# Kernel optimization log

Measured on AMD Instinct MI355X. Metric: run time of the kernel, lower is better.

The kernel has to match this reference:

```python
import jax, jax.numpy as jnp
import numpy as np

B, S, D, H = 4, 2048, 1024, 16
DH = D // H


def setup_inputs() -> dict:
    key = jax.random.key(0)
    kq, kk, kv, kw, kb = jax.random.split(key, 5)
    queries = jax.random.normal(kq, (B, S, D), dtype=jnp.float32)
    keys = jax.random.normal(kk, (B, S, D), dtype=jnp.float32)
    values = jax.random.normal(kv, (B, S, D), dtype=jnp.float32)
    # True = masked-out padding position; mask the last 64 keys of batch 0
    kpm = np.zeros((B, S), dtype=bool)
    kpm[0, -64:] = True
    key_padding_mask = jnp.asarray(kpm)
    W_O = jax.random.normal(kw, (D, D), dtype=jnp.float32) / np.sqrt(D)
    b_O = jax.random.normal(kb, (D,), dtype=jnp.float32) * 0.01
    return {"queries": queries, "keys": keys, "values": values,
            "key_padding_mask": key_padding_mask, "W_O": W_O, "b_O": b_O}


def reference(queries, keys, values, key_padding_mask, W_O, b_O):
    batch, len_q, d_model = queries.shape
    len_k = keys.shape[1]
    # [B, H, S, DH]
    q = queries.reshape(batch, len_q, H, DH).transpose(0, 2, 1, 3)
    k = keys.reshape(batch, len_k, H, DH).transpose(0, 2, 1, 3)
    v = values.reshape(batch, len_k, H, DH).transpose(0, 2, 1, 3)
    sim = jnp.einsum('bhqd,bhkd->bhqk', q, k) / jnp.sqrt(jnp.float32(DH))
    neg_inf = jnp.finfo(sim.dtype).min
    # padding mask: True means masked
    sim = jnp.where(key_padding_mask[:, None, None, :], neg_inf, sim)
    # causal mask (is_causal=True)
    causal = jnp.tril(jnp.ones((len_q, len_k), dtype=bool))
    sim = jnp.where(causal[None, None], sim, neg_inf)
    attn = jax.nn.softmax(sim, axis=-1)
    out = jnp.einsum('bhqk,bhkd->bhqd', attn, v)  # [B, H, Sq, DH]
    out = out.transpose(0, 2, 1, 3).reshape(batch, len_q, d_model)
    return out @ W_O.T + b_O
```

## Files before the change

### kernel.cpp

```cpp
#include <hip/hip_runtime.h>
#include <hip/hip_bf16.h>

#define B_ 4
#define S_ 2048
#define D_ 1024
#define H_ 16
#define DH_ 64

typedef __attribute__((ext_vector_type(8))) short bf16x8;
typedef __attribute__((ext_vector_type(4))) float f32x4;
typedef __attribute__((ext_vector_type(16))) float f32x16;
typedef __attribute__((ext_vector_type(2))) int v2i;
typedef unsigned int uint32;

__device__ __forceinline__ unsigned short f2bf(float f) {
  unsigned int u = __float_as_uint(f);
  u += 0x7FFFu + ((u >> 16) & 1u);
  return (unsigned short)(u >> 16);
}

__device__ __forceinline__ uint32 pk2(float lo, float hi) {
  return __builtin_amdgcn_perm(__float_as_uint(hi), __float_as_uint(lo), 0x07060302u);
}

__device__ __forceinline__ float half_add(float v) {
  v2i r = __builtin_amdgcn_permlane32_swap(__float_as_int(v), __float_as_int(v), false, false);
  return __int_as_float(r[0]) + __int_as_float(r[1]);
}

__global__ void prep_kernel(const float* __restrict__ k, const float* __restrict__ w,
                            const int* __restrict__ kpm, const float* __restrict__ v,
                            ushort* __restrict__ Kb, ushort* __restrict__ Wb,
                            float* __restrict__ MF, int* __restrict__ anyM,
                            ushort* __restrict__ Vt) {
  __shared__ ushort tile[64][68];
  const int bid = blockIdx.x;
  const int t = threadIdx.x;
  if (bid < 8192) {
    int i = bid * 256 + t;
    float4 a = ((const float4*)k)[i];
    ushort4 r;
    r.x = f2bf(a.x); r.y = f2bf(a.y); r.z = f2bf(a.z); r.w = f2bf(a.w);
    ((ushort4*)Kb)[i] = r;
  } else if (bid < 9216) {
    int i = (bid - 8192) * 256 + t;
    float4 a = ((const float4*)w)[i];
    ushort4 r;
    r.x = f2bf(a.x); r.y = f2bf(a.y); r.z = f2bf(a.z); r.w = f2bf(a.w);
    ((ushort4*)Wb)[i] = r;
  } else if (bid < 9248) {
    int i = (bid - 9216) * 256 + t;
    int m = kpm[i];
    MF[i] = m ? -1e30f : 0.0f;
    unsigned long long bal = __ballot(m != 0);
    if ((i & 63) == 0) anyM[i >> 6] = (bal != 0ull) ? 1 : 0;
  } else {
    int bx = bid - 9248;
    int bh = bx >> 5;
    int s0 = (bx & 31) << 6;
    int b = bh >> 4, h = bh & 15;
#pragma unroll
    for (int it = 0; it < 16; ++it) {
      int r = it * 4 + (t >> 6);
      int c = t & 63;
      float x = v[(size_t)(b * S_ + s0 + r) * D_ + h * DH_ + c];
      tile[r][c] = f2bf(x);
    }
    __syncthreads();
#pragma unroll
    for (int it = 0; it < 16; ++it) {
      int d = it * 4 + (t >> 6);
      int s = t & 63;
      Vt[(size_t)(bh * DH_ + d) * S_ + s0 + s] = tile[s][d];
    }
  }
}

__global__ __launch_bounds__(256, 2) void attn_fwd(
    const float* __restrict__ q, const ushort* __restrict__ Kb,
    const ushort* __restrict__ Vt, const float* __restrict__ MF,
    const int* __restrict__ anyM, ushort* __restrict__ AO) {
  __shared__ ushort Klds[2][2][64 * 64];
  __shared__ ushort Vlds[2][2][64 * 64];

  const int b = blockIdx.z, h = blockIdx.y;
  const int xx = blockIdx.x;
  const int tid = threadIdx.x;
  const int wv = tid >> 6, ln = tid & 63;
  const int q32 = ln & 31;
  const int hi = ln >> 5;
  const int l7 = ln & 7, l3 = ln >> 3;
  const float SC = 0.18033688011112042f;
  const int cr4 = 4 * hi;

  const ushort* Kg = Kb + (size_t)b * S_ * D_ + h * DH_;
  const ushort* Vg = Vt + (size_t)((b * H_ + h) * DH_) * S_;

  bf16x8 kst[4], vst[4];
  const int wrow0 = 16 * wv + l3;
  const int wss = (l7 ^ l3) * 8;

  f32x16 zz;
#pragma unroll
  for (int i = 0; i < 16; ++i) zz[i] = 0.f;

  auto loadTile = [&](int kt) {
#pragma unroll
    for (int hh = 0; hh < 2; ++hh)
#pragma unroll
      for (int p = 0; p < 2; ++p) {
        int row = wrow0 + 8 * p;
        kst[2 * hh + p] = *(const bf16x8*)(Kg + (size_t)(kt * 128 + hh * 64 + row) * D_ + l7 * 8);
        vst[2 * hh + p] = *(const bf16x8*)(Vg + (size_t)row * S_ + kt * 128 + hh * 64 + l7 * 8);
      }
  };
  auto writeTile = [&](int buf) {
#pragma unroll
    for (int hh = 0; hh < 2; ++hh)
#pragma unroll
      for (int p = 0; p < 2; ++p) {
        int row = wrow0 + 8 * p;
        *(bf16x8*)(&Klds[buf][hh][row * 64 + wss]) = kst[2 * hh + p];
        *(bf16x8*)(&Vlds[buf][hh][row * 64 + wss]) = vst[2 * hh + p];
      }
  };
  auto packTile = [&](const f32x16& pv, bf16x8* out) {
#pragma unroll
    for (int kk = 0; kk < 2; ++kk) {
      uint32 a  = pk2(pv[8 * kk + 0], pv[8 * kk + 1]);
      uint32 c  = pk2(pv[8 * kk + 2], pv[8 * kk + 3]);
      uint32 bb = pk2(pv[8 * kk + 4], pv[8 * kk + 5]);
      uint32 dd = pk2(pv[8 * kk + 6], pv[8 * kk + 7]);
      v2i r0 = __builtin_amdgcn_permlane32_swap((int)a, (int)bb, false, false);
      v2i r1 = __builtin_amdgcn_permlane32_swap((int)c, (int)dd, false, false);
      union { uint32 u[4]; bf16x8 v; } w;
      w.u[0] = (uint32)r0[0]; w.u[1] = (uint32)r1[0];
      w.u[2] = (uint32)r0[1]; w.u[3] = (uint32)r1[1];
      out[kk] = w.v;
    }
  };

  for (int half = 0; half < 2; ++half) {
    const int q0 = (half ? (15 - xx) : xx) * 128;
    const int qw0 = q0 + wv * 32;
    const int qb = qw0 >> 5;

    bf16x8 qf[4];
    {
      const float* qp = q + (size_t)(b * S_ + qw0 + q32) * D_ + h * DH_ + hi * 8;
#pragma unroll
      for (int j = 0; j < 4; ++j) {
        float4 x0 = *(const float4*)(qp + 16 * j);
        float4 x1 = *(const float4*)(qp + 16 * j + 4);
        bf16x8 t;
        t[0] = (short)f2bf(x0.x * SC); t[1] = (short)f2bf(x0.y * SC);
        t[2] = (short)f2bf(x0.z * SC); t[3] = (short)f2bf(x0.w * SC);
        t[4] = (short)f2bf(x1.x * SC); t[5] = (short)f2bf(x1.y * SC);
        t[6] = (short)f2bf(x1.z * SC); t[7] = (short)f2bf(x1.w * SC);
        qf[j] = t;
      }
    }

    f32x16 ot0, ot1;
#pragma unroll
    for (int i = 0; i < 16; ++i) { ot0[i] = 0.f; ot1[i] = 0.f; }
    float l_run = 0.f;

    auto full64 = [&](int cur, int hh) {
      const ushort* Kl = &Klds[cur][hh][0];
      const ushort* Vl = &Vlds[cur][hh][0];
      f32x16 s0v, s1v;
#pragma unroll
      for (int j = 0; j < 4; ++j) {
        bf16x8 kf = *(const bf16x8*)(&Kl[q32 * 64 + (((2 * j + hi) ^ l7) * 8)]);
        s0v = __builtin_amdgcn_mfma_f32_32x32x16_bf16(kf, qf[j], j ? s0v : zz, 0, 0, 0);
      }
#pragma unroll
      for (int j = 0; j < 4; ++j) {
        bf16x8 kf = *(const bf16x8*)(&Kl[(32 + q32) * 64 + (((2 * j + hi) ^ l7) * 8)]);
        s1v = __builtin_amdgcn_mfma_f32_32x32x16_bf16(kf, qf[j], j ? s1v : zz, 0, 0, 0);
      }
      float rsa = 0.f, rsb = 0.f;
#pragma unroll
      for (int r = 0; r < 16; ++r) {
        float p0 = __builtin_amdgcn_exp2f(s0v[r]); s0v[r] = p0;
        float p1 = __builtin_amdgcn_exp2f(s1v[r]); s1v[r] = p1;
        if (r & 1) { rsb += p0; rsb += p1; } else { rsa += p0; rsa += p1; }
      }
      l_run += half_add(rsa + rsb);

      bf16x8 pa[4];
      packTile(s0v, &pa[0]);
      packTile(s1v, &pa[2]);
#pragma unroll
      for (int dt = 0; dt < 2; ++dt) {
        f32x16& ot = dt ? ot1 : ot0;
        const int rowb = (dt * 32 + q32) * 64;
        bf16x8 v0 = *(const bf16x8*)(&Vl[rowb + (((0 + hi) ^ l7) * 8)]);
        ot = __builtin_amdgcn_mfma_f32_32x32x16_bf16(v0, pa[0], ot, 0, 0, 0);
        bf16x8 v1 = *(const bf16x8*)(&Vl[rowb + (((2 + hi) ^ l7) * 8)]);
        ot = __builtin_amdgcn_mfma_f32_32x32x16_bf16(v1, pa[1], ot, 0, 0, 0);
        bf16x8 v2 = *(const bf16x8*)(&Vl[rowb + (((4 + hi) ^ l7) * 8)]);
        ot = __builtin_amdgcn_mfma_f32_32x32x16_bf16(v2, pa[2], ot, 0, 0, 0);
        bf16x8 v3 = *(const bf16x8*)(&Vl[rowb + (((6 + hi) ^ l7) * 8)]);
        ot = __builtin_amdgcn_mfma_f32_32x32x16_bf16(v3, pa[3], ot, 0, 0, 0);
      }
    };

    auto generic64 = [&](int t64, int cur, int hh) {
      const int k0 = t64 * 64;
      const ushort* Kl = &Klds[cur][hh][0];
      const ushort* Vl = &Vlds[cur][hh][0];
      const bool a0 = (2 * t64) <= qb, a1 = (2 * t64 + 1) <= qb;
      if (!(a0 || a1)) return;
      const bool dg0 = (2 * t64) == qb, dg1 = (2 * t64 + 1) == qb;
      const int flag = anyM[b * 32 + t64];

      f32x16 s0v, s1v;
      if (a0) {
#pragma unroll
        for (int j = 0; j < 4; ++j) {
          bf16x8 kf = *(const bf16x8*)(&Kl[q32 * 64 + (((2 * j + hi) ^ l7) * 8)]);
          s0v = __builtin_amdgcn_mfma_f32_32x32x16_bf16(kf, qf[j], j ? s0v : zz, 0, 0, 0);
        }
      }
      if (a1) {
#pragma unroll
        for (int j = 0; j < 4; ++j) {
          bf16x8 kf = *(const bf16x8*)(&Kl[(32 + q32) * 64 + (((2 * j + hi) ^ l7) * 8)]);
          s1v = __builtin_amdgcn_mfma_f32_32x32x16_bf16(kf, qf[j], j ? s1v : zz, 0, 0, 0);
        }
      }

      float rsa = 0.f, rsb = 0.f;
      if (a0) {
#pragma unroll
        for (int r = 0; r < 16; ++r) {
          int cr = (r & 3) + 8 * (r >> 2) + cr4;
          float s = s0v[r];
          if (flag) s += MF[b * S_ + k0 + cr];
          if (dg0 && cr > q32) s = -3.0e38f;
          float p = __builtin_amdgcn_exp2f(s);
          s0v[r] = p;
          if (r & 1) rsb += p; else rsa += p;
        }
      }
      if (a1) {
#pragma unroll
        for (int r = 0; r < 16; ++r) {
          int cr = (r & 3) + 8 * (r >> 2) + cr4;
          float s = s1v[r];
          if (flag) s += MF[b * S_ + k0 + 32 + cr];
          if (dg1 && cr > q32) s = -3.0e38f;
          float p = __builtin_amdgcn_exp2f(s);
          s1v[r] = p;
          if (r & 1) rsb += p; else rsa += p;
        }
      }
      l_run += half_add(rsa + rsb);

      bf16x8 pa[4];
      if (a0) packTile(s0v, &pa[0]);
      if (a1) packTile(s1v, &pa[2]);

#pragma unroll
      for (int dt = 0; dt < 2; ++dt) {
        f32x16& ot = dt ? ot1 : ot0;
        const int rowb = (dt * 32 + q32) * 64;
        if (a0) {
          bf16x8 v0 = *(const bf16x8*)(&Vl[rowb + (((0 + hi) ^ l7) * 8)]);
          ot = __builtin_amdgcn_mfma_f32_32x32x16_bf16(v0, pa[0], ot, 0, 0, 0);
          bf16x8 v1 = *(const bf16x8*)(&Vl[rowb + (((2 + hi) ^ l7) * 8)]);
          ot = __builtin_amdgcn_mfma_f32_32x32x16_bf16(v1, pa[1], ot, 0, 0, 0);
        }
        if (a1) {
          bf16x8 v2 = *(const bf16x8*)(&Vl[rowb + (((4 + hi) ^ l7) * 8)]);
          ot = __builtin_amdgcn_mfma_f32_32x32x16_bf16(v2, pa[2], ot, 0, 0, 0);
          bf16x8 v3 = *(const bf16x8*)(&Vl[rowb + (((6 + hi) ^ l7) * 8)]);
          ot = __builtin_amdgcn_mfma_f32_32x32x16_bf16(v3, pa[3], ot, 0, 0, 0);
        }
      }
    };

    const int M = (q0 >> 7) + 1;
    loadTile(0);
    writeTile(0);
    if (M > 1) loadTile(1);
    __syncthreads();

    for (int tt = 0; tt < M; ++tt) {
      const int cur = tt & 1;
      if (tt + 1 < M) writeTile(cur ^ 1);
      if (tt + 2 < M) loadTile(tt + 2);
      if (tt < M - 1) {
        const int f0 = anyM[b * 32 + 2 * tt] | anyM[b * 32 + 2 * tt + 1];
        if (f0) { generic64(2 * tt, cur, 0); generic64(2 * tt + 1, cur, 1); }
        else { full64(cur, 0); full64(cur, 1); }
      } else {
        generic64(2 * tt, cur, 0);
        generic64(2 * tt + 1, cur, 1);
      }
      __syncthreads();
    }

    const float inv = __builtin_amdgcn_rcpf(l_run);
    ushort* tb = ((ushort*)Klds) + wv * 2048;
#pragma unroll
    for (int dt = 0; dt < 2; ++dt) {
      const f32x16& ot = dt ? ot1 : ot0;
#pragma unroll
      for (int rp = 0; rp < 8; ++rp) {
        int r0 = rp * 2;
        int d0 = dt * 32 + (r0 & 3) + 8 * (r0 >> 2) + cr4;
        uint32 w = pk2(ot[r0] * inv, ot[r0 + 1] * inv);
        int e = q32 * 64 + (((d0 >> 3) ^ (q32 & 7)) * 8) + (d0 & 7);
        *(uint32*)(&tb[e]) = w;
      }
    }
    __syncthreads();
#pragma unroll
    for (int it = 0; it < 4; ++it) {
      int qq = it * 8 + l3;
      bf16x8 val = *(const bf16x8*)(&tb[qq * 64 + ((l7 ^ (qq & 7)) * 8)]);
      *(bf16x8*)(AO + (size_t)(b * S_ + qw0 + qq) * D_ + h * DH_ + l7 * 8) = val;
    }
    __syncthreads();
  }
}

__global__ __launch_bounds__(256, 2) void gemm_out(
    const ushort* __restrict__ A, const ushort* __restrict__ Wb,
    const float* __restrict__ bO, float* __restrict__ out) {
  __shared__ ushort Al[128 * 64];
  __shared__ ushort Wl[128 * 64];
  const int n0 = blockIdx.x * 128;
  const int m0 = blockIdx.y * 128;
  const int tid = threadIdx.x;
  const int wv = tid >> 6, ln = tid & 63;
  const int r16 = ln & 15, g = ln >> 4;
  const int wm = wv >> 1, wn = wv & 1;
  const int trow = tid >> 3, tslot = tid & 7;
  f32x4 acc[4][4] = {};

  for (int kk = 0; kk < D_; kk += 64) {
#pragma unroll
    for (int p = 0; p < 4; ++p) {
      int row = trow + 32 * p;
      int soff = (tslot ^ (row & 7)) * 8;
      *(bf16x8*)(&Al[row * 64 + soff]) =
          *(const bf16x8*)(A + (size_t)(m0 + row) * D_ + kk + tslot * 8);
      *(bf16x8*)(&Wl[row * 64 + soff]) =
          *(const bf16x8*)(Wb + (size_t)(n0 + row) * D_ + kk + tslot * 8);
    }
    __syncthreads();
#pragma unroll
    for (int hh = 0; hh < 2; ++hh) {
      bf16x8 af[4], wf[4];
#pragma unroll
      for (int m = 0; m < 4; ++m) {
        int row = 64 * wm + 16 * m + r16;
        af[m] = *(const bf16x8*)(&Al[row * 64 + (((4 * hh + g) ^ (row & 7)) * 8)]);
      }
#pragma unroll
      for (int n = 0; n < 4; ++n) {
        int row = 64 * wn + 16 * n + r16;
        wf[n] = *(const bf16x8*)(&Wl[row * 64 + (((4 * hh + g) ^ (row & 7)) * 8)]);
      }
#pragma unroll
      for (int m = 0; m < 4; ++m)
#pragma unroll
        for (int n = 0; n < 4; ++n)
          acc[m][n] = __builtin_amdgcn_mfma_f32_16x16x32_bf16(af[m], wf[n], acc[m][n], 0, 0, 0);
    }
    __syncthreads();
  }

#pragma unroll
  for (int n = 0; n < 4; ++n) {
    float bb = bO[n0 + 64 * wn + 16 * n + r16];
#pragma unroll
    for (int m = 0; m < 4; ++m) {
#pragma unroll
      for (int j = 0; j < 4; ++j) {
        out[(size_t)(m0 + 64 * wm + 16 * m + 4 * g + j) * D_ + n0 + 64 * wn + 16 * n + r16] =
            acc[m][n][j] + bb;
      }
    }
  }
}

extern "C" void kernel_launch(void* const* d_in, const int* in_sizes, int n_in,
                              void* d_out, int out_size, void* d_ws, size_t ws_size,
                              hipStream_t stream) {
  const float* q = (const float*)d_in[0];
  const float* k = (const float*)d_in[1];
  const float* v = (const float*)d_in[2];
  const int* kpm = (const int*)d_in[3];
  const float* W = (const float*)d_in[4];
  const float* bO = (const float*)d_in[5];

  char* ws = (char*)d_ws;
  const size_t SZ = (size_t)B_ * S_ * D_ * 2;
  ushort* Kb = (ushort*)ws;
  ushort* Vt = (ushort*)(ws + SZ);
  ushort* AO = (ushort*)(ws + 2 * SZ);
  ushort* Wb = (ushort*)(ws + 3 * SZ);
  float* MF = (float*)(ws + 3 * SZ + (size_t)D_ * D_ * 2);
  int* anyM = (int*)(ws + 3 * SZ + (size_t)D_ * D_ * 2 + (size_t)B_ * S_ * 4);

  prep_kernel<<<11296, 256, 0, stream>>>(k, W, kpm, v, Kb, Wb, MF, anyM, Vt);
  attn_fwd<<<dim3(8, H_, B_), 256, 0, stream>>>(q, Kb, Vt, MF, anyM, AO);
  gemm_out<<<dim3(8, 64), 256, 0, stream>>>(AO, Wb, bO, (float*)d_out);
}
```

Baseline: 110.7 us.

## Double-buffer output GEMM via register prefetch and defer row-sum reduction

Measured after the change: 108.0 us. 2.4% less time.

```diff
diff --git a/kernel.cpp b/kernel.cpp
--- a/kernel.cpp
+++ b/kernel.cpp
@@ -187,7 +187,7 @@
         float p1 = __builtin_amdgcn_exp2f(s1v[r]); s1v[r] = p1;
         if (r & 1) { rsb += p0; rsb += p1; } else { rsa += p0; rsa += p1; }
       }
-      l_run += half_add(rsa + rsb);
+      l_run += rsa + rsb;
 
       bf16x8 pa[4];
       packTile(s0v, &pa[0]);
@@ -257,7 +257,7 @@
           if (r & 1) rsb += p; else rsa += p;
         }
       }
-      l_run += half_add(rsa + rsb);
+      l_run += rsa + rsb;
 
       bf16x8 pa[4];
       if (a0) packTile(s0v, &pa[0]);
@@ -303,7 +303,7 @@
       __syncthreads();
     }
 
-    const float inv = __builtin_amdgcn_rcpf(l_run);
+    const float inv = __builtin_amdgcn_rcpf(half_add(l_run));
     ushort* tb = ((ushort*)Klds) + wv * 2048;
 #pragma unroll
     for (int dt = 0; dt < 2; ++dt) {
@@ -331,8 +331,8 @@
 __global__ __launch_bounds__(256, 2) void gemm_out(
     const ushort* __restrict__ A, const ushort* __restrict__ Wb,
     const float* __restrict__ bO, float* __restrict__ out) {
-  __shared__ ushort Al[128 * 64];
-  __shared__ ushort Wl[128 * 64];
+  __shared__ ushort Al[2][128 * 64];
+  __shared__ ushort Wl[2][128 * 64];
   const int n0 = blockIdx.x * 128;
   const int m0 = blockIdx.y * 128;
   const int tid = threadIdx.x;
@@ -341,30 +341,48 @@
   const int wm = wv >> 1, wn = wv & 1;
   const int trow = tid >> 3, tslot = tid & 7;
   f32x4 acc[4][4] = {};
-
-  for (int kk = 0; kk < D_; kk += 64) {
+  bf16x8 ast[4], wst[4];
+
+  auto stageReg = [&](int kc) {
+    const int kk = kc * 64;
+#pragma unroll
+    for (int p = 0; p < 4; ++p) {
+      int row = trow + 32 * p;
+      ast[p] = *(const bf16x8*)(A + (size_t)(m0 + row) * D_ + kk + tslot * 8);
+      wst[p] = *(const bf16x8*)(Wb + (size_t)(n0 + row) * D_ + kk + tslot * 8);
+    }
+  };
+  auto writeL = [&](int buf) {
 #pragma unroll
     for (int p = 0; p < 4; ++p) {
       int row = trow + 32 * p;
       int soff = (tslot ^ (row & 7)) * 8;
-      *(bf16x8*)(&Al[row * 64 + soff]) =
-          *(const bf16x8*)(A + (size_t)(m0 + row) * D_ + kk + tslot * 8);
-      *(bf16x8*)(&Wl[row * 64 + soff]) =
-          *(const bf16x8*)(Wb + (size_t)(n0 + row) * D_ + kk + tslot * 8);
-    }
-    __syncthreads();
+      *(bf16x8*)(&Al[buf][row * 64 + soff]) = ast[p];
+      *(bf16x8*)(&Wl[buf][row * 64 + soff]) = wst[p];
+    }
+  };
+
+  stageReg(0);
+  writeL(0);
+  stageReg(1);
+  __syncthreads();
+
+  for (int kc = 0; kc < 16; ++kc) {
+    const int cur = kc & 1;
+    if (kc + 1 < 16) writeL(cur ^ 1);
+    if (kc + 2 < 16) stageReg(kc + 2);
 #pragma unroll
     for (int hh = 0; hh < 2; ++hh) {
       bf16x8 af[4], wf[4];
 #pragma unroll
       for (int m = 0; m < 4; ++m) {
         int row = 64 * wm + 16 * m + r16;
-        af[m] = *(const bf16x8*)(&Al[row * 64 + (((4 * hh + g) ^ (row & 7)) * 8)]);
+        af[m] = *(const bf16x8*)(&Al[cur][row * 64 + (((4 * hh + g) ^ (row & 7)) * 8)]);
       }
 #pragma unroll
       for (int n = 0; n < 4; ++n) {
         int row = 64 * wn + 16 * n + r16;
-        wf[n] = *(const bf16x8*)(&Wl[row * 64 + (((4 * hh + g) ^ (row & 7)) * 8)]);
+        wf[n] = *(const bf16x8*)(&Wl[cur][row * 64 + (((4 * hh + g) ^ (row & 7)) * 8)]);
       }
 #pragma unroll
       for (int m = 0; m < 4; ++m)
```
